# Kernel optimization log

Hardware: AMD Instinct MI355X
Metric: run time of the kernel (lower is better)

Reference implementation:

```python
import jax, jax.numpy as jnp
import numpy as np

RBF_START = 0.0
RBF_END = 8.0
RBF_STEPS = 32
OUT_SIZE = 64
ENERGY_SCALE = 0.01


def setup_inputs() -> dict:
    key = jax.random.key(0)
    k1, k2, k3, k4 = jax.random.split(key, 4)
    L, R = 512, 4096
    return {
        "lig_feat": jax.random.normal(k1, (L, RBF_STEPS, OUT_SIZE), dtype=jnp.float32),
        "rec_feat": jax.random.normal(k2, (R, RBF_STEPS, OUT_SIZE), dtype=jnp.float32),
        "lig_coord": jax.random.normal(k3, (L, 3), dtype=jnp.float32),
        "rec_coord": jax.random.normal(k4, (R, 3), dtype=jnp.float32),
    }


def reference(lig_feat, rec_feat, lig_coord, rec_coord):
    # attention coefficients: contract over (rbf step 'e' kept, feature 'f' summed)
    atn_coefs = jnp.einsum('lef,ref->lre', lig_feat, rec_feat)  # [L,R,steps]
    # pairwise distances [L,R]
    diff = lig_coord[:, None, :] - rec_coord[None, :, :]
    dists = jnp.sqrt(jnp.sum(diff * diff, axis=-1))
    # RBF encoding [L,R,steps]
    mu = jnp.linspace(RBF_START, RBF_END, RBF_STEPS, dtype=dists.dtype)
    sigma = (RBF_START - RBF_END) / RBF_STEPS
    z = (dists[..., None] - mu) / sigma
    rbfs = jnp.exp(-(z * z))
    # weighted energy sum (scalar)
    U = jnp.sum(atn_coefs * rbfs) * ENERGY_SCALE
    return U
```

## Files before the change

kernel.cpp:

```cpp
#include <hip/hip_runtime.h>
#include <math.h>

#define LN 512
#define RN 4096
#define EN 32
#define FN 64

#define BLT 128
#define BRT 128
#define EH  4

#define K16LOG2E 23.083120654223415f
#define MU_STEP (8.0f / 31.0f)

typedef _Float16 half8 __attribute__((ext_vector_type(8)));
typedef __attribute__((ext_vector_type(4))) float f32x4;

#define APLANE 0
#define BPLANE (128 * 128)
#define LDS_BYTES (2 * 128 * 128)

#define WS_LIG 0
#define WS_REC (2u * 1024 * 1024)
#define WS_PART (18u * 1024 * 1024)

#define LCHUNKS (LN * EN * 8)
#define RCHUNKS (RN * EN * 8)

typedef const __attribute__((address_space(1))) unsigned int* gas_ptr;
typedef __attribute__((address_space(3))) unsigned int* las_ptr;
#define GL16(g, l) __builtin_amdgcn_global_load_lds((gas_ptr)(g), (las_ptr)(l), 16, 0, 0)

__global__ __launch_bounds__(256) void ff_convert(
    const float* __restrict__ lig_feat, const float* __restrict__ rec_feat,
    unsigned short* __restrict__ lig_swz, unsigned short* __restrict__ rec_swz)
{
    int idx = blockIdx.x * 256 + threadIdx.x;
    const float* src;
    unsigned short* dst;
    if (idx < LCHUNKS) {
        src = lig_feat; dst = lig_swz;
    } else {
        idx -= LCHUNKS;
        src = rec_feat; dst = rec_swz;
    }
    const int row = idx >> 8;
    const int e   = (idx >> 3) & 31;
    const int gf  = idx & 7;

    const float* s = src + (((size_t)row * EN + e) * FN + gf * 8);
    const float4 v0 = *(const float4*)s;
    const float4 v1 = *(const float4*)(s + 4);

    const unsigned short q0 = __builtin_bit_cast(unsigned short, (_Float16)v0.x);
    const unsigned short q1 = __builtin_bit_cast(unsigned short, (_Float16)v0.y);
    const unsigned short q2 = __builtin_bit_cast(unsigned short, (_Float16)v0.z);
    const unsigned short q3 = __builtin_bit_cast(unsigned short, (_Float16)v0.w);
    const unsigned short q4 = __builtin_bit_cast(unsigned short, (_Float16)v1.x);
    const unsigned short q5 = __builtin_bit_cast(unsigned short, (_Float16)v1.y);
    const unsigned short q6 = __builtin_bit_cast(unsigned short, (_Float16)v1.z);
    const unsigned short q7 = __builtin_bit_cast(unsigned short, (_Float16)v1.w);
    uint4 o;
    o.x = (unsigned)q0 | ((unsigned)q1 << 16);
    o.y = (unsigned)q2 | ((unsigned)q3 << 16);
    o.z = (unsigned)q4 | ((unsigned)q5 << 16);
    o.w = (unsigned)q6 | ((unsigned)q7 << 16);

    const size_t dpos = (((size_t)row * EN + e) * 8 + (gf ^ (row & 7))) * 8;
    *(uint4*)(dst + dpos) = o;
}

__global__ __launch_bounds__(512, 1) void ff_mfma(
    const unsigned short* __restrict__ lig_swz,
    const unsigned short* __restrict__ rec_swz,
    const float* __restrict__ lig_coord,
    const float* __restrict__ rec_coord,
    float* __restrict__ partial)
{
    __shared__ char lds[LDS_BYTES];

    const int tid  = threadIdx.x;
    const int lane = tid & 63;
    const int w    = tid >> 6;
    const int wl   = (w & 3) * 2;
    const int wr   = (w >> 2) * 4;
    const int lrow = lane & 15;
    const int lk   = lane >> 4;

    const int l0 = blockIdx.y * BLT;
    const int r0 = blockIdx.x * BRT;
    const int e0 = blockIdx.z * EH;

    int soff[2];
    #pragma unroll
    for (int k = 0; k < 2; ++k) {
        const int idx = k * 512 + tid;
        soff[k] = (idx >> 3) * (EN * 128) + (idx & 7) * 16;
    }
    const char* ligb = (const char*)lig_swz + (size_t)l0 * (EN * 128);
    const char* recb = (const char*)rec_swz + (size_t)r0 * (EN * 128);

    float rcx[4], rcy[4], rcz[4];
    #pragma unroll
    for (int tj = 0; tj < 4; ++tj) {
        const int r = r0 + (wr + tj) * 16 + lrow;
        rcx[tj] = rec_coord[r * 3 + 0];
        rcy[tj] = rec_coord[r * 3 + 1];
        rcz[tj] = rec_coord[r * 3 + 2];
    }
    float d[2][4][4];
    #pragma unroll
    for (int ti = 0; ti < 2; ++ti) {
        #pragma unroll
        for (int i = 0; i < 4; ++i) {
            const int l = l0 + (wl + ti) * 16 + lk * 4 + i;
            const float lx = lig_coord[l * 3 + 0];
            const float ly = lig_coord[l * 3 + 1];
            const float lz = lig_coord[l * 3 + 2];
            #pragma unroll
            for (int tj = 0; tj < 4; ++tj) {
                const float dx = lx - rcx[tj];
                const float dy = ly - rcy[tj];
                const float dz = lz - rcz[tj];
                d[ti][tj][i] = sqrtf(fmaf(dx, dx, fmaf(dy, dy, dz * dz)));
            }
        }
    }

    float usum = 0.0f;

    for (int ee = 0; ee < EH; ++ee) {
        const int e = e0 + ee;
        const int ebyte = e * 128;

        __syncthreads();

        #pragma unroll
        for (int k = 0; k < 2; ++k) {
            const int idx = k * 512 + tid;
            GL16(ligb + soff[k] + ebyte, lds + APLANE + idx * 16);
        }
        #pragma unroll
        for (int k = 0; k < 2; ++k) {
            const int idx = k * 512 + tid;
            GL16(recb + soff[k] + ebyte, lds + BPLANE + idx * 16);
        }
        __syncthreads();

        f32x4 acc[2][4];
        #pragma unroll
        for (int ti = 0; ti < 2; ++ti)
            #pragma unroll
            for (int tj = 0; tj < 4; ++tj)
                acc[ti][tj] = (f32x4){0.f, 0.f, 0.f, 0.f};

        #pragma unroll
        for (int kc = 0; kc < 2; ++kc) {
            const int inrow = (kc * 64 + lk * 16) ^ ((lrow & 7) << 4);
            half8 af[2], bf_[4];
            #pragma unroll
            for (int t = 0; t < 2; ++t) {
                const int arow = (wl + t) * 16 + lrow;
                af[t] = *(const half8*)(lds + APLANE + arow * 128 + inrow);
            }
            #pragma unroll
            for (int t = 0; t < 4; ++t) {
                const int brow = (wr + t) * 16 + lrow;
                bf_[t] = *(const half8*)(lds + BPLANE + brow * 128 + inrow);
            }
            #pragma unroll
            for (int ti = 0; ti < 2; ++ti) {
                #pragma unroll
                for (int tj = 0; tj < 4; ++tj) {
                    acc[ti][tj] = __builtin_amdgcn_mfma_f32_16x16x32_f16(
                        af[ti], bf_[tj], acc[ti][tj], 0, 0, 0);
                }
            }
        }

        const float mu = (float)e * MU_STEP;
        #pragma unroll
        for (int ti = 0; ti < 2; ++ti) {
            #pragma unroll
            for (int tj = 0; tj < 4; ++tj) {
                #pragma unroll
                for (int i = 0; i < 4; ++i) {
                    const float t = d[ti][tj][i] - mu;
                    const float wgt = __builtin_amdgcn_exp2f(-K16LOG2E * t * t);
                    usum = fmaf(acc[ti][tj][i], wgt, usum);
                }
            }
        }
    }

    __syncthreads();
    float* red = (float*)lds;
    red[tid] = usum;
    __syncthreads();
    #pragma unroll
    for (int st = 256; st > 0; st >>= 1) {
        if (tid < st) red[tid] += red[tid + st];
        __syncthreads();
    }
    if (tid == 0) {
        const int bidx = (blockIdx.z * gridDim.y + blockIdx.y) * gridDim.x + blockIdx.x;
        partial[bidx] = red[0];
    }
}

__global__ __launch_bounds__(256) void ff_reduce(
    const float* __restrict__ partial, float* __restrict__ out, int n)
{
    __shared__ float s[256];
    float v = 0.0f;
    for (int i = threadIdx.x; i < n; i += 256) v += partial[i];
    s[threadIdx.x] = v;
    __syncthreads();
    #pragma unroll
    for (int st = 128; st > 0; st >>= 1) {
        if (threadIdx.x < st) s[threadIdx.x] += s[threadIdx.x + st];
        __syncthreads();
    }
    if (threadIdx.x == 0) out[0] = s[0] * 0.01f;
}

extern "C" void kernel_launch(void* const* d_in, const int* in_sizes, int n_in,
                              void* d_out, int out_size, void* d_ws, size_t ws_size,
                              hipStream_t stream)
{
    const float* lig_feat  = (const float*)d_in[0];
    const float* rec_feat  = (const float*)d_in[1];
    const float* lig_coord = (const float*)d_in[2];
    const float* rec_coord = (const float*)d_in[3];
    float* out = (float*)d_out;

    unsigned short* lig_swz = (unsigned short*)((char*)d_ws + WS_LIG);
    unsigned short* rec_swz = (unsigned short*)((char*)d_ws + WS_REC);
    float* partial          = (float*)((char*)d_ws + WS_PART);

    const int nChunks = LCHUNKS + RCHUNKS;
    ff_convert<<<nChunks / 256, 256, 0, stream>>>(lig_feat, rec_feat, lig_swz, rec_swz);

    const dim3 grid(RN / BRT, LN / BLT, EN / EH);
    ff_mfma<<<grid, dim3(512), 0, stream>>>(lig_swz, rec_swz, lig_coord, rec_coord, partial);

    const int nPartial = (RN / BRT) * (LN / BLT) * (EN / EH);
    ff_reduce<<<1, 256, 0, stream>>>(partial, out, nPartial);
}
```

Measured before the change: 44.38 us.

## Load MFMA operands directly from global memory, dropping LDS staging and swizzle

```diff
diff --git a/kernel.cpp b/kernel.cpp
--- a/kernel.cpp
+++ b/kernel.cpp
@@ -6,52 +6,38 @@
 #define EN 32
 #define FN 64
 
-#define BLT 128
+#define BLT 64
 #define BRT 128
-#define EH  4
+#define EHB 8
 
 #define K16LOG2E 23.083120654223415f
 #define MU_STEP (8.0f / 31.0f)
 
 typedef _Float16 half8 __attribute__((ext_vector_type(8)));
 typedef __attribute__((ext_vector_type(4))) float f32x4;
-
-#define APLANE 0
-#define BPLANE (128 * 128)
-#define LDS_BYTES (2 * 128 * 128)
 
 #define WS_LIG 0
 #define WS_REC (2u * 1024 * 1024)
 #define WS_PART (18u * 1024 * 1024)
 
-#define LCHUNKS (LN * EN * 8)
-#define RCHUNKS (RN * EN * 8)
-
-typedef const __attribute__((address_space(1))) unsigned int* gas_ptr;
-typedef __attribute__((address_space(3))) unsigned int* las_ptr;
-#define GL16(g, l) __builtin_amdgcn_global_load_lds((gas_ptr)(g), (las_ptr)(l), 16, 0, 0)
+#define LELEM (LN * EN * FN)
+#define RELEM (RN * EN * FN)
 
 __global__ __launch_bounds__(256) void ff_convert(
     const float* __restrict__ lig_feat, const float* __restrict__ rec_feat,
-    unsigned short* __restrict__ lig_swz, unsigned short* __restrict__ rec_swz)
-{
-    int idx = blockIdx.x * 256 + threadIdx.x;
+    unsigned short* __restrict__ lig_h, unsigned short* __restrict__ rec_h)
+{
+    size_t idx = (size_t)blockIdx.x * 256 + threadIdx.x;
     const float* src;
     unsigned short* dst;
-    if (idx < LCHUNKS) {
-        src = lig_feat; dst = lig_swz;
+    if (idx < LELEM / 8) {
+        src = lig_feat; dst = lig_h;
     } else {
-        idx -= LCHUNKS;
-        src = rec_feat; dst = rec_swz;
-    }
-    const int row = idx >> 8;
-    const int e   = (idx >> 3) & 31;
-    const int gf  = idx & 7;
-
-    const float* s = src + (((size_t)row * EN + e) * FN + gf * 8);
-    const float4 v0 = *(const float4*)s;
-    const float4 v1 = *(const float4*)(s + 4);
-
+        idx -= LELEM / 8;
+        src = rec_feat; dst = rec_h;
+    }
+    const float4 v0 = *(const float4*)(src + idx * 8);
+    const float4 v1 = *(const float4*)(src + idx * 8 + 4);
     const unsigned short q0 = __builtin_bit_cast(unsigned short, (_Float16)v0.x);
     const unsigned short q1 = __builtin_bit_cast(unsigned short, (_Float16)v0.y);
     const unsigned short q2 = __builtin_bit_cast(unsigned short, (_Float16)v0.z);
@@ -65,40 +51,43 @@
     o.y = (unsigned)q2 | ((unsigned)q3 << 16);
     o.z = (unsigned)q4 | ((unsigned)q5 << 16);
     o.w = (unsigned)q6 | ((unsigned)q7 << 16);
-
-    const size_t dpos = (((size_t)row * EN + e) * 8 + (gf ^ (row & 7))) * 8;
-    *(uint4*)(dst + dpos) = o;
-}
-
-__global__ __launch_bounds__(512, 1) void ff_mfma(
-    const unsigned short* __restrict__ lig_swz,
-    const unsigned short* __restrict__ rec_swz,
+    *(uint4*)(dst + idx * 8) = o;
+}
+
+__global__ __launch_bounds__(256, 1) void ff_mfma(
+    const unsigned short* __restrict__ lig_h,
+    const unsigned short* __restrict__ rec_h,
     const float* __restrict__ lig_coord,
     const float* __restrict__ rec_coord,
     float* __restrict__ partial)
 {
-    __shared__ char lds[LDS_BYTES];
+    __shared__ float red[256];
 
     const int tid  = threadIdx.x;
     const int lane = tid & 63;
     const int w    = tid >> 6;
-    const int wl   = (w & 3) * 2;
-    const int wr   = (w >> 2) * 4;
+    const int wl   = (w & 1) * 2;
+    const int wr   = (w >> 1) * 4;
     const int lrow = lane & 15;
     const int lk   = lane >> 4;
 
     const int l0 = blockIdx.y * BLT;
     const int r0 = blockIdx.x * BRT;
-    const int e0 = blockIdx.z * EH;
-
-    int soff[2];
-    #pragma unroll
-    for (int k = 0; k < 2; ++k) {
-        const int idx = k * 512 + tid;
-        soff[k] = (idx >> 3) * (EN * 128) + (idx & 7) * 16;
-    }
-    const char* ligb = (const char*)lig_swz + (size_t)l0 * (EN * 128);
-    const char* recb = (const char*)rec_swz + (size_t)r0 * (EN * 128);
+    const int e0 = blockIdx.z * EHB;
+
+    int voffA[2], voffB[4];
+    #pragma unroll
+    for (int ti = 0; ti < 2; ++ti) {
+        const int arow = l0 + (wl + ti) * 16 + lrow;
+        voffA[ti] = arow * 4096 + e0 * 128 + lk * 16;
+    }
+    #pragma unroll
+    for (int tj = 0; tj < 4; ++tj) {
+        const int brow = r0 + (wr + tj) * 16 + lrow;
+        voffB[tj] = brow * 4096 + e0 * 128 + lk * 16;
+    }
+    const char* ligb = (const char*)lig_h;
+    const char* recb = (const char*)rec_h;
 
     float rcx[4], rcy[4], rcz[4];
     #pragma unroll
@@ -129,24 +118,8 @@
 
     float usum = 0.0f;
 
-    for (int ee = 0; ee < EH; ++ee) {
-        const int e = e0 + ee;
-        const int ebyte = e * 128;
-
-        __syncthreads();
-
-        #pragma unroll
-        for (int k = 0; k < 2; ++k) {
-            const int idx = k * 512 + tid;
-            GL16(ligb + soff[k] + ebyte, lds + APLANE + idx * 16);
-        }
-        #pragma unroll
-        for (int k = 0; k < 2; ++k) {
-            const int idx = k * 512 + tid;
-            GL16(recb + soff[k] + ebyte, lds + BPLANE + idx * 16);
-        }
-        __syncthreads();
-
+    #pragma unroll
+    for (int ee = 0; ee < EHB; ++ee) {
         f32x4 acc[2][4];
         #pragma unroll
         for (int ti = 0; ti < 2; ++ti)
@@ -156,18 +129,14 @@
 
         #pragma unroll
         for (int kc = 0; kc < 2; ++kc) {
-            const int inrow = (kc * 64 + lk * 16) ^ ((lrow & 7) << 4);
+            const int imm = ee * 128 + kc * 64;
             half8 af[2], bf_[4];
             #pragma unroll
-            for (int t = 0; t < 2; ++t) {
-                const int arow = (wl + t) * 16 + lrow;
-                af[t] = *(const half8*)(lds + APLANE + arow * 128 + inrow);
-            }
-            #pragma unroll
-            for (int t = 0; t < 4; ++t) {
-                const int brow = (wr + t) * 16 + lrow;
-                bf_[t] = *(const half8*)(lds + BPLANE + brow * 128 + inrow);
-            }
+            for (int ti = 0; ti < 2; ++ti)
+                af[ti] = *(const half8*)(ligb + voffA[ti] + imm);
+            #pragma unroll
+            for (int tj = 0; tj < 4; ++tj)
+                bf_[tj] = *(const half8*)(recb + voffB[tj] + imm);
             #pragma unroll
             for (int ti = 0; ti < 2; ++ti) {
                 #pragma unroll
@@ -178,7 +147,7 @@
             }
         }
 
-        const float mu = (float)e * MU_STEP;
+        const float mu = (float)(e0 + ee) * MU_STEP;
         #pragma unroll
         for (int ti = 0; ti < 2; ++ti) {
             #pragma unroll
@@ -193,12 +162,10 @@
         }
     }
 
-    __syncthreads();
-    float* red = (float*)lds;
     red[tid] = usum;
     __syncthreads();
     #pragma unroll
-    for (int st = 256; st > 0; st >>= 1) {
+    for (int st = 128; st > 0; st >>= 1) {
         if (tid < st) red[tid] += red[tid + st];
         __syncthreads();
     }
@@ -234,16 +201,16 @@
     const float* rec_coord = (const float*)d_in[3];
     float* out = (float*)d_out;
 
-    unsigned short* lig_swz = (unsigned short*)((char*)d_ws + WS_LIG);
-    unsigned short* rec_swz = (unsigned short*)((char*)d_ws + WS_REC);
-    float* partial          = (float*)((char*)d_ws + WS_PART);
-
-    const int nChunks = LCHUNKS + RCHUNKS;
-    ff_convert<<<nChunks / 256, 256, 0, stream>>>(lig_feat, rec_feat, lig_swz, rec_swz);
-
-    const dim3 grid(RN / BRT, LN / BLT, EN / EH);
-    ff_mfma<<<grid, dim3(512), 0, stream>>>(lig_swz, rec_swz, lig_coord, rec_coord, partial);
-
-    const int nPartial = (RN / BRT) * (LN / BLT) * (EN / EH);
+    unsigned short* lig_h = (unsigned short*)((char*)d_ws + WS_LIG);
+    unsigned short* rec_h = (unsigned short*)((char*)d_ws + WS_REC);
+    float* partial        = (float*)((char*)d_ws + WS_PART);
+
+    const int nThreads8 = (LELEM + RELEM) / 8;
+    ff_convert<<<nThreads8 / 256, 256, 0, stream>>>(lig_feat, rec_feat, lig_h, rec_h);
+
+    const dim3 grid(RN / BRT, LN / BLT, EN / EHB);
+    ff_mfma<<<grid, dim3(256), 0, stream>>>(lig_h, rec_h, lig_coord, rec_coord, partial);
+
+    const int nPartial = (RN / BRT) * (LN / BLT) * (EN / EHB);
     ff_reduce<<<1, 256, 0, stream>>>(partial, out, nPartial);
 }
```

After: 63.66 us. 43.4% more time.

## Double-buffer LDS feature slices and double the RBF steps per block

Applied to the files above, without the earlier changes.

```diff
diff --git a/kernel.cpp b/kernel.cpp
--- a/kernel.cpp
+++ b/kernel.cpp
@@ -8,7 +8,7 @@
 
 #define BLT 128
 #define BRT 128
-#define EH  4
+#define EH  8
 
 #define K16LOG2E 23.083120654223415f
 #define MU_STEP (8.0f / 31.0f)
@@ -16,9 +16,8 @@
 typedef _Float16 half8 __attribute__((ext_vector_type(8)));
 typedef __attribute__((ext_vector_type(4))) float f32x4;
 
-#define APLANE 0
-#define BPLANE (128 * 128)
-#define LDS_BYTES (2 * 128 * 128)
+#define BUFBYTES 32768
+#define BPLANE   16384
 
 #define WS_LIG 0
 #define WS_REC (2u * 1024 * 1024)
@@ -77,7 +76,7 @@
     const float* __restrict__ rec_coord,
     float* __restrict__ partial)
 {
-    __shared__ char lds[LDS_BYTES];
+    __shared__ char lds[2 * BUFBYTES];
 
     const int tid  = threadIdx.x;
     const int lane = tid & 63;
@@ -100,6 +99,16 @@
     const char* ligb = (const char*)lig_swz + (size_t)l0 * (EN * 128);
     const char* recb = (const char*)rec_swz + (size_t)r0 * (EN * 128);
 
+#define STAGE(b, e_) do {                                                   \
+        const int ebyte_ = (e_) * 128;                                      \
+        _Pragma("unroll")                                                   \
+        for (int k_ = 0; k_ < 2; ++k_) {                                    \
+            const int idx_ = k_ * 512 + tid;                                \
+            GL16(ligb + soff[k_] + ebyte_, lds + (b) * BUFBYTES + idx_ * 16);            \
+            GL16(recb + soff[k_] + ebyte_, lds + (b) * BUFBYTES + BPLANE + idx_ * 16);   \
+        }                                                                   \
+    } while (0)
+
     float rcx[4], rcy[4], rcz[4];
     #pragma unroll
     for (int tj = 0; tj < 4; ++tj) {
@@ -127,25 +136,18 @@
         }
     }
 
+    STAGE(0, e0);
+    __syncthreads();
+
     float usum = 0.0f;
 
     for (int ee = 0; ee < EH; ++ee) {
-        const int e = e0 + ee;
-        const int ebyte = e * 128;
-
-        __syncthreads();
-
-        #pragma unroll
-        for (int k = 0; k < 2; ++k) {
-            const int idx = k * 512 + tid;
-            GL16(ligb + soff[k] + ebyte, lds + APLANE + idx * 16);
-        }
-        #pragma unroll
-        for (int k = 0; k < 2; ++k) {
-            const int idx = k * 512 + tid;
-            GL16(recb + soff[k] + ebyte, lds + BPLANE + idx * 16);
-        }
-        __syncthreads();
+        const int cur = ee & 1;
+        const int e   = e0 + ee;
+
+        if (ee + 1 < EH) STAGE(cur ^ 1, e + 1);
+
+        const char* base = lds + cur * BUFBYTES;
 
         f32x4 acc[2][4];
         #pragma unroll
@@ -161,12 +163,12 @@
             #pragma unroll
             for (int t = 0; t < 2; ++t) {
                 const int arow = (wl + t) * 16 + lrow;
-                af[t] = *(const half8*)(lds + APLANE + arow * 128 + inrow);
+                af[t] = *(const half8*)(base + arow * 128 + inrow);
             }
             #pragma unroll
             for (int t = 0; t < 4; ++t) {
                 const int brow = (wr + t) * 16 + lrow;
-                bf_[t] = *(const half8*)(lds + BPLANE + brow * 128 + inrow);
+                bf_[t] = *(const half8*)(base + BPLANE + brow * 128 + inrow);
             }
             #pragma unroll
             for (int ti = 0; ti < 2; ++ti) {
@@ -191,9 +193,10 @@
                 }
             }
         }
-    }
-
-    __syncthreads();
+
+        __syncthreads();
+    }
+
     float* red = (float*)lds;
     red[tid] = usum;
     __syncthreads();
@@ -206,6 +209,7 @@
         const int bidx = (blockIdx.z * gridDim.y + blockIdx.y) * gridDim.x + blockIdx.x;
         partial[bidx] = red[0];
     }
+#undef STAGE
 }
 
 __global__ __launch_bounds__(256) void ff_reduce(
```

New measurement: 40.02 us. -9.8%, faster.
